# Optimization experiments

Measured on AMD Instinct MI355X. Metric: run time of the kernel, lower is better.

Reference implementation:

```python
import jax, jax.numpy as jnp
import numpy as np

# Irrep dims for irreps 0e, 1o, 2e: 2l+1
IRREP_DIMS = (1, 3, 5)
B, N, C_IN, C_OUT = 8, 4096, 256, 256
FEAT = sum(IRREP_DIMS)  # 9


def setup_inputs() -> dict:
    key = jax.random.key(0)
    kx, k0, k1, k2 = jax.random.split(key, 4)
    std = C_IN ** -0.5  # VarianceScaling(fan_in) init
    return {
        "x": jax.random.normal(kx, (B, N, C_IN, FEAT), dtype=jnp.float32),
        "w0": jax.random.normal(k0, (C_IN, C_OUT), dtype=jnp.float32) * std,
        "w1": jax.random.normal(k1, (C_IN, C_OUT), dtype=jnp.float32) * std,
        "w2": jax.random.normal(k2, (C_IN, C_OUT), dtype=jnp.float32) * std,
    }


def reference(x, w0, w1, w2):
    # EquivariantLinear with mix_channels=True:
    #  - axis_to_mul merges the channel axis into irrep multiplicity, so each
    #    irrep block x[..., k, m] (k = channel/mul index, m = 2l+1 component)
    #    is contracted over k with a per-irrep weight w_l [mul_in, mul_out],
    #    scaled by path_weight = 1/sqrt(fan_in) (single path per output irrep).
    #  - mul_to_axis splits the multiplicity back into the channel axis.
    # Block-diagonal structure: one small matmul per matching irrep pair.
    mul_in = x.shape[-2]
    pw = jnp.asarray(mul_in, x.dtype) ** -0.5  # path_weight (1/sqrt fan_in)
    outs = []
    offset = 0
    for w, d in zip((w0, w1, w2), IRREP_DIMS):
        xl = jax.lax.slice_in_dim(x, offset, offset + d, axis=-1)  # [B,N,C,d]
        outs.append(pw * jnp.einsum('bnkm,kc->bncm', xl, w))
        offset += d
    return jnp.concatenate(outs, axis=-1)  # [B, N, C_out, 9]
```

## Files before the change

### kernel.cpp

```cpp
#include <hip/hip_runtime.h>


typedef float f32x4 __attribute__((ext_vector_type(4)));
typedef float f32x4u __attribute__((ext_vector_type(4), aligned(4)));
typedef short s16x8 __attribute__((ext_vector_type(8)));

#define POSB 16
#define XS_KS 264
#define XS_MS (POSB * XS_KS)
#define SMEM_BYTES (9 * XS_MS * 2)
#define STG_ROW 148

__device__ __forceinline__ unsigned short f2bf(float f) {
  unsigned u = __float_as_uint(f);
  return (unsigned short)((u + 0x7FFFu + ((u >> 16) & 1u)) >> 16);
}

__device__ __forceinline__ unsigned cvt_pk_bf16(float lo, float hi) {
  unsigned r;
  asm("v_cvt_pk_bf16_f32 %0, %1, %2" : "=v"(r) : "v"(lo), "v"(hi));
  return r;
}

__global__ void prep_w(const float* __restrict__ w0, const float* __restrict__ w1,
                       const float* __restrict__ w2, unsigned short* __restrict__ wt) {
  const int b = blockIdx.x;
  const int irr = b / 16;
  const int tile = b % 16;
  const int k0 = (tile >> 2) << 6;
  const int c0 = (tile & 3) << 6;
  const float* w = (irr == 0) ? w0 : ((irr == 1) ? w1 : w2);
  __shared__ float lt[64 * 65];
  const int t = threadIdx.x;
#pragma unroll
  for (int i = 0; i < 16; ++i) {
    int e = t + (i << 8);
    int kk = e >> 6, cc = e & 63;
    lt[cc * 65 + kk] = w[(k0 + kk) * 256 + (c0 + cc)];
  }
  __syncthreads();
#pragma unroll
  for (int i = 0; i < 16; ++i) {
    int e = t + (i << 8);
    int cc = e >> 6, kk = e & 63;
    wt[irr * 65536 + (c0 + cc) * 256 + (k0 + kk)] = f2bf(lt[cc * 65 + kk] * 0.0625f);
  }
}

__global__ __launch_bounds__(512, 4) void eqlin_main(
    const float* __restrict__ x, const unsigned short* __restrict__ wt,
    float* __restrict__ out) {
  extern __shared__ char smem[];
  unsigned short* xs = reinterpret_cast<unsigned short*>(smem);

  const int t = threadIdx.x;
  const long long blk = blockIdx.x;
  const float* xb = x + blk * (POSB * 2304);

  {
    f32x4u va[8], vb[8];
    float vc[8];
#pragma unroll
    for (int i = 0; i < 8; ++i) {
      const float* s = xb + (t + (i << 9)) * 9;
      va[i] = *reinterpret_cast<const f32x4u*>(s);
      vb[i] = *reinterpret_cast<const f32x4u*>(s + 4);
      vc[i] = s[8];
    }
#pragma unroll
    for (int i = 0; i < 8; ++i) {
      const int u = t + (i << 9);
      const int pos = u >> 8;
      const int k = u & 255;
      unsigned short* base = xs + pos * XS_KS + k;
      unsigned p01 = cvt_pk_bf16(va[i][0], va[i][1]);
      unsigned p23 = cvt_pk_bf16(va[i][2], va[i][3]);
      unsigned p45 = cvt_pk_bf16(vb[i][0], vb[i][1]);
      unsigned p67 = cvt_pk_bf16(vb[i][2], vb[i][3]);
      base[0 * XS_MS] = (unsigned short)p01;
      base[1 * XS_MS] = (unsigned short)(p01 >> 16);
      base[2 * XS_MS] = (unsigned short)p23;
      base[3 * XS_MS] = (unsigned short)(p23 >> 16);
      base[4 * XS_MS] = (unsigned short)p45;
      base[5 * XS_MS] = (unsigned short)(p45 >> 16);
      base[6 * XS_MS] = (unsigned short)p67;
      base[7 * XS_MS] = (unsigned short)(p67 >> 16);
      base[8 * XS_MS] = f2bf(vc[i]);
    }
  }
  __syncthreads();

  const int w = t >> 6;
  const int l = t & 63;
  const int cr = l & 15;
  const int kg = (l >> 4) << 3;
  const int c0 = w << 5;

  const unsigned short* xsA = xs + cr * XS_KS + kg;
  const unsigned short* wtB = wt + (c0 + cr) * 256 + kg;

  f32x4 accA[4][2];
#pragma unroll
  for (int m = 0; m < 4; ++m)
#pragma unroll
    for (int ct = 0; ct < 2; ++ct) accA[m][ct] = (f32x4){0.f, 0.f, 0.f, 0.f};

#pragma unroll 2
  for (int ks = 0; ks < 8; ++ks) {
    const int kk = ks << 5;
    s16x8 b00 = *reinterpret_cast<const s16x8*>(wtB + kk);
    s16x8 b01 = *reinterpret_cast<const s16x8*>(wtB + 4096 + kk);
    s16x8 b10 = *reinterpret_cast<const s16x8*>(wtB + 65536 + kk);
    s16x8 b11 = *reinterpret_cast<const s16x8*>(wtB + 65536 + 4096 + kk);
    {
      s16x8 a = *reinterpret_cast<const s16x8*>(xsA + kk);
      accA[0][0] = __builtin_amdgcn_mfma_f32_16x16x32_bf16(a, b00, accA[0][0], 0, 0, 0);
      accA[0][1] = __builtin_amdgcn_mfma_f32_16x16x32_bf16(a, b01, accA[0][1], 0, 0, 0);
    }
#pragma unroll
    for (int m = 1; m < 4; ++m) {
      s16x8 a = *reinterpret_cast<const s16x8*>(xsA + m * XS_MS + kk);
      accA[m][0] = __builtin_amdgcn_mfma_f32_16x16x32_bf16(a, b10, accA[m][0], 0, 0, 0);
      accA[m][1] = __builtin_amdgcn_mfma_f32_16x16x32_bf16(a, b11, accA[m][1], 0, 0, 0);
    }
  }

  f32x4 accB[5][2];
#pragma unroll
  for (int m = 0; m < 5; ++m)
#pragma unroll
    for (int ct = 0; ct < 2; ++ct) accB[m][ct] = (f32x4){0.f, 0.f, 0.f, 0.f};

#pragma unroll 2
  for (int ks = 0; ks < 8; ++ks) {
    const int kk = ks << 5;
    s16x8 b20 = *reinterpret_cast<const s16x8*>(wtB + 2 * 65536 + kk);
    s16x8 b21 = *reinterpret_cast<const s16x8*>(wtB + 2 * 65536 + 4096 + kk);
#pragma unroll
    for (int m = 0; m < 5; ++m) {
      s16x8 a = *reinterpret_cast<const s16x8*>(xsA + (m + 4) * XS_MS + kk);
      accB[m][0] = __builtin_amdgcn_mfma_f32_16x16x32_bf16(a, b20, accB[m][0], 0, 0, 0);
      accB[m][1] = __builtin_amdgcn_mfma_f32_16x16x32_bf16(a, b21, accB[m][1], 0, 0, 0);
    }
  }
  __syncthreads();

  float* stgw = reinterpret_cast<float*>(smem) + w * (POSB * STG_ROW);
  const int posb = (l >> 4) << 2;
  f32x4* o4 = reinterpret_cast<f32x4*>(out) + blk * 9216 + w * 72;

#pragma unroll
  for (int ct = 0; ct < 2; ++ct) {
#pragma unroll
    for (int m = 0; m < 9; ++m) {
#pragma unroll
      for (int j = 0; j < 4; ++j) {
        float v = (m < 4) ? accA[m][ct][j] : accB[m - 4][ct][j];
        stgw[(posb + j) * STG_ROW + cr * 9 + m] = v;
      }
    }
    asm volatile("s_waitcnt lgkmcnt(0)" ::: "memory");
#pragma unroll
    for (int q = 0; q < 9; ++q) {
      const int e = l + (q << 6);
      const int pos = (int)((unsigned)e / 36u);
      const int rem = e - pos * 36;
      f32x4 v = *reinterpret_cast<const f32x4*>(stgw + pos * STG_ROW + (rem << 2));
      __builtin_nontemporal_store(v, &o4[pos * 576 + ct * 36 + rem]);
    }
    asm volatile("s_waitcnt lgkmcnt(0)" ::: "memory");
  }
}

extern "C" void kernel_launch(void* const* d_in, const int* in_sizes, int n_in,
                              void* d_out, int out_size, void* d_ws, size_t ws_size,
                              hipStream_t stream) {
  const float* x = (const float*)d_in[0];
  const float* w0 = (const float*)d_in[1];
  const float* w1 = (const float*)d_in[2];
  const float* w2 = (const float*)d_in[3];
  unsigned short* wt = (unsigned short*)d_ws;
  float* out = (float*)d_out;

  prep_w<<<48, 256, 0, stream>>>(w0, w1, w2, wt);

  (void)hipFuncSetAttribute(reinterpret_cast<const void*>(eqlin_main),
                            hipFuncAttributeMaxDynamicSharedMemorySize, SMEM_BYTES);
  eqlin_main<<<2048, 512, SMEM_BYTES, stream>>>(x, wt, out);
}
```

Before: 162.8 us.

## Pack two irrep components per MFMA row tile and halve positions per block

Each block now handles 8 positions with 256 threads, and each wave covers 64 output channels instead of 32. The 16-row MFMA A tile packs two different m-components (8 positions each) that share the same weight, so wasted row padding is removed and the number of MFMAs drops from 18 to 6 tiles per channel tile. The output staging is reorganised to match, and the grid doubles. This raises register pressure (24 accumulators) and lowers launch bounds, in return for fewer MFMAs and fewer redundant weight loads.

```diff
diff --git a/kernel.cpp b/kernel.cpp
--- a/kernel.cpp
+++ b/kernel.cpp
@@ -5,11 +5,11 @@
 typedef float f32x4u __attribute__((ext_vector_type(4), aligned(4)));
 typedef short s16x8 __attribute__((ext_vector_type(8)));
 
-#define POSB 16
+#define POSB 8
 #define XS_KS 264
 #define XS_MS (POSB * XS_KS)
 #define SMEM_BYTES (9 * XS_MS * 2)
-#define STG_ROW 148
+#define STG_ROW 292
 
 __device__ __forceinline__ unsigned short f2bf(float f) {
   unsigned u = __float_as_uint(f);
@@ -47,7 +47,7 @@
   }
 }
 
-__global__ __launch_bounds__(512, 4) void eqlin_main(
+__global__ __launch_bounds__(256, 3) void eqlin_main(
     const float* __restrict__ x, const unsigned short* __restrict__ wt,
     float* __restrict__ out) {
   extern __shared__ char smem[];
@@ -62,14 +62,14 @@
     float vc[8];
 #pragma unroll
     for (int i = 0; i < 8; ++i) {
-      const float* s = xb + (t + (i << 9)) * 9;
+      const float* s = xb + (t + (i << 8)) * 9;
       va[i] = *reinterpret_cast<const f32x4u*>(s);
       vb[i] = *reinterpret_cast<const f32x4u*>(s + 4);
       vc[i] = s[8];
     }
 #pragma unroll
     for (int i = 0; i < 8; ++i) {
-      const int u = t + (i << 9);
+      const int u = t + (i << 8);
       const int pos = u >> 8;
       const int k = u & 255;
       unsigned short* base = xs + pos * XS_KS + k;
@@ -94,79 +94,84 @@
   const int l = t & 63;
   const int cr = l & 15;
   const int kg = (l >> 4) << 3;
-  const int c0 = w << 5;
+  const int c0 = w << 6;
 
-  const unsigned short* xsA = xs + cr * XS_KS + kg;
+  const bool hi = (cr >= 8);
+  const unsigned short* xrow = xs + (cr & 7) * XS_KS + kg;
+  const unsigned short* xa[6] = {
+      xrow + 0 * XS_MS,
+      xrow + (hi ? 2 : 1) * XS_MS,
+      xrow + 3 * XS_MS,
+      xrow + (hi ? 5 : 4) * XS_MS,
+      xrow + (hi ? 7 : 6) * XS_MS,
+      xrow + 8 * XS_MS,
+  };
+
   const unsigned short* wtB = wt + (c0 + cr) * 256 + kg;
 
-  f32x4 accA[4][2];
+  f32x4 acc[4][6];
 #pragma unroll
-  for (int m = 0; m < 4; ++m)
+  for (int ct = 0; ct < 4; ++ct)
 #pragma unroll
-    for (int ct = 0; ct < 2; ++ct) accA[m][ct] = (f32x4){0.f, 0.f, 0.f, 0.f};
+    for (int T = 0; T < 6; ++T) acc[ct][T] = (f32x4){0.f, 0.f, 0.f, 0.f};
 
 #pragma unroll 2
   for (int ks = 0; ks < 8; ++ks) {
     const int kk = ks << 5;
-    s16x8 b00 = *reinterpret_cast<const s16x8*>(wtB + kk);
-    s16x8 b01 = *reinterpret_cast<const s16x8*>(wtB + 4096 + kk);
-    s16x8 b10 = *reinterpret_cast<const s16x8*>(wtB + 65536 + kk);
-    s16x8 b11 = *reinterpret_cast<const s16x8*>(wtB + 65536 + 4096 + kk);
-    {
-      s16x8 a = *reinterpret_cast<const s16x8*>(xsA + kk);
-      accA[0][0] = __builtin_amdgcn_mfma_f32_16x16x32_bf16(a, b00, accA[0][0], 0, 0, 0);
-      accA[0][1] = __builtin_amdgcn_mfma_f32_16x16x32_bf16(a, b01, accA[0][1], 0, 0, 0);
-    }
+    s16x8 a0 = *reinterpret_cast<const s16x8*>(xa[0] + kk);
+    s16x8 a1 = *reinterpret_cast<const s16x8*>(xa[1] + kk);
+    s16x8 a2 = *reinterpret_cast<const s16x8*>(xa[2] + kk);
+    s16x8 a3 = *reinterpret_cast<const s16x8*>(xa[3] + kk);
+    s16x8 a4 = *reinterpret_cast<const s16x8*>(xa[4] + kk);
+    s16x8 a5 = *reinterpret_cast<const s16x8*>(xa[5] + kk);
 #pragma unroll
-    for (int m = 1; m < 4; ++m) {
-      s16x8 a = *reinterpret_cast<const s16x8*>(xsA + m * XS_MS + kk);
-      accA[m][0] = __builtin_amdgcn_mfma_f32_16x16x32_bf16(a, b10, accA[m][0], 0, 0, 0);
-      accA[m][1] = __builtin_amdgcn_mfma_f32_16x16x32_bf16(a, b11, accA[m][1], 0, 0, 0);
-    }
-  }
-
-  f32x4 accB[5][2];
-#pragma unroll
-  for (int m = 0; m < 5; ++m)
-#pragma unroll
-    for (int ct = 0; ct < 2; ++ct) accB[m][ct] = (f32x4){0.f, 0.f, 0.f, 0.f};
-
-#pragma unroll 2
-  for (int ks = 0; ks < 8; ++ks) {
-    const int kk = ks << 5;
-    s16x8 b20 = *reinterpret_cast<const s16x8*>(wtB + 2 * 65536 + kk);
-    s16x8 b21 = *reinterpret_cast<const s16x8*>(wtB + 2 * 65536 + 4096 + kk);
-#pragma unroll
-    for (int m = 0; m < 5; ++m) {
-      s16x8 a = *reinterpret_cast<const s16x8*>(xsA + (m + 4) * XS_MS + kk);
-      accB[m][0] = __builtin_amdgcn_mfma_f32_16x16x32_bf16(a, b20, accB[m][0], 0, 0, 0);
-      accB[m][1] = __builtin_amdgcn_mfma_f32_16x16x32_bf16(a, b21, accB[m][1], 0, 0, 0);
+    for (int ct = 0; ct < 4; ++ct) {
+      const unsigned short* wc = wtB + ct * 4096 + kk;
+      s16x8 b0 = *reinterpret_cast<const s16x8*>(wc);
+      s16x8 b1 = *reinterpret_cast<const s16x8*>(wc + 65536);
+      s16x8 b2 = *reinterpret_cast<const s16x8*>(wc + 131072);
+      acc[ct][0] = __builtin_amdgcn_mfma_f32_16x16x32_bf16(a0, b0, acc[ct][0], 0, 0, 0);
+      acc[ct][1] = __builtin_amdgcn_mfma_f32_16x16x32_bf16(a1, b1, acc[ct][1], 0, 0, 0);
+      acc[ct][2] = __builtin_amdgcn_mfma_f32_16x16x32_bf16(a2, b1, acc[ct][2], 0, 0, 0);
+      acc[ct][3] = __builtin_amdgcn_mfma_f32_16x16x32_bf16(a3, b2, acc[ct][3], 0, 0, 0);
+      acc[ct][4] = __builtin_amdgcn_mfma_f32_16x16x32_bf16(a4, b2, acc[ct][4], 0, 0, 0);
+      acc[ct][5] = __builtin_amdgcn_mfma_f32_16x16x32_bf16(a5, b2, acc[ct][5], 0, 0, 0);
     }
   }
   __syncthreads();
 
   float* stgw = reinterpret_cast<float*>(smem) + w * (POSB * STG_ROW);
-  const int posb = (l >> 4) << 2;
-  f32x4* o4 = reinterpret_cast<f32x4*>(out) + blk * 9216 + w * 72;
+  const int g = l >> 4;
+  const int posb = (g & 1) << 2;
+
+  const int pAt[6] = {0, 1, 3, 4, 6, 8};
+  const int pBt[6] = {0, 2, 3, 5, 7, 8};
+
+  f32x4* o4 = reinterpret_cast<f32x4*>(out);
 
 #pragma unroll
-  for (int ct = 0; ct < 2; ++ct) {
+  for (int h = 0; h < 2; ++h) {
 #pragma unroll
-    for (int m = 0; m < 9; ++m) {
+    for (int ch = 0; ch < 2; ++ch) {
 #pragma unroll
-      for (int j = 0; j < 4; ++j) {
-        float v = (m < 4) ? accA[m][ct][j] : accB[m - 4][ct][j];
-        stgw[(posb + j) * STG_ROW + cr * 9 + m] = v;
+      for (int T = 0; T < 6; ++T) {
+        const int m = (g < 2) ? pAt[T] : pBt[T];
+        if (g < 2 || pAt[T] != pBt[T]) {
+#pragma unroll
+          for (int j = 0; j < 4; ++j)
+            stgw[(posb + j) * STG_ROW + ((ch << 4) + cr) * 9 + m] = acc[2 * h + ch][T][j];
+        }
       }
     }
     asm volatile("s_waitcnt lgkmcnt(0)" ::: "memory");
 #pragma unroll
     for (int q = 0; q < 9; ++q) {
       const int e = l + (q << 6);
-      const int pos = (int)((unsigned)e / 36u);
-      const int rem = e - pos * 36;
+      const int pos = (int)((unsigned)e / 72u);
+      const int rem = e - pos * 72;
       f32x4 v = *reinterpret_cast<const f32x4*>(stgw + pos * STG_ROW + (rem << 2));
-      __builtin_nontemporal_store(v, &o4[pos * 576 + ct * 36 + rem]);
+      __builtin_nontemporal_store(
+          v, &o4[(blk * POSB + pos) * 576 + w * 144 + h * 72 + rem]);
     }
     asm volatile("s_waitcnt lgkmcnt(0)" ::: "memory");
   }
@@ -186,5 +191,5 @@
 
   (void)hipFuncSetAttribute(reinterpret_cast<const void*>(eqlin_main),
                             hipFuncAttributeMaxDynamicSharedMemorySize, SMEM_BYTES);
-  eqlin_main<<<2048, 512, SMEM_BYTES, stream>>>(x, wt, out);
+  eqlin_main<<<4096, 256, SMEM_BYTES, stream>>>(x, wt, out);
 }
```

After: 280.0 us. +72.0%, slower.

## Make main kernel persistent over four tiles with double-buffered LDS prefetch

Applied to the files above, without the earlier changes.

Each block now processes four 16-position tiles instead of one, with two LDS buffers. The global loads for the next tile are issued before the MFMA loop of the current tile and staged into the other buffer after the output is written, so memory latency overlaps compute. The grid shrinks to 512 blocks, LDS use doubles, and launch bounds drop to 2 blocks per CU. That lowers occupancy and raises register pressure from holding prefetched tiles in registers.

```diff
diff --git a/kernel.cpp b/kernel.cpp
--- a/kernel.cpp
+++ b/kernel.cpp
@@ -8,8 +8,11 @@
 #define POSB 16
 #define XS_KS 264
 #define XS_MS (POSB * XS_KS)
-#define SMEM_BYTES (9 * XS_MS * 2)
+#define BUF_BYTES (9 * XS_MS * 2)
+#define SMEM_BYTES (2 * BUF_BYTES)
 #define STG_ROW 148
+#define NT 4
+#define TILE_FLOATS (POSB * 2304)
 
 __device__ __forceinline__ unsigned short f2bf(float f) {
   unsigned u = __float_as_uint(f);
@@ -20,6 +23,10 @@
   unsigned r;
   asm("v_cvt_pk_bf16_f32 %0, %1, %2" : "=v"(r) : "v"(lo), "v"(hi));
   return r;
+}
+
+__device__ __forceinline__ void bar_nodrain() {
+  asm volatile("s_waitcnt lgkmcnt(0)\n\ts_barrier" ::: "memory");
 }
 
 __global__ void prep_w(const float* __restrict__ w0, const float* __restrict__ w1,
@@ -47,128 +54,151 @@
   }
 }
 
-__global__ __launch_bounds__(512, 4) void eqlin_main(
+__device__ __forceinline__ void load8(const float* __restrict__ xb, int t,
+                                      f32x4u* va, f32x4u* vb, float* vc) {
+#pragma unroll
+  for (int i = 0; i < 8; ++i) {
+    const float* s = xb + (t + (i << 9)) * 9;
+    va[i] = *reinterpret_cast<const f32x4u*>(s);
+    vb[i] = *reinterpret_cast<const f32x4u*>(s + 4);
+    vc[i] = s[8];
+  }
+}
+
+__device__ __forceinline__ void stage8(unsigned short* __restrict__ xs, int t,
+                                       const f32x4u* va, const f32x4u* vb,
+                                       const float* vc) {
+#pragma unroll
+  for (int i = 0; i < 8; ++i) {
+    const int u = t + (i << 9);
+    const int pos = u >> 8;
+    const int k = u & 255;
+    unsigned short* base = xs + pos * XS_KS + k;
+    unsigned p01 = cvt_pk_bf16(va[i][0], va[i][1]);
+    unsigned p23 = cvt_pk_bf16(va[i][2], va[i][3]);
+    unsigned p45 = cvt_pk_bf16(vb[i][0], vb[i][1]);
+    unsigned p67 = cvt_pk_bf16(vb[i][2], vb[i][3]);
+    base[0 * XS_MS] = (unsigned short)p01;
+    base[1 * XS_MS] = (unsigned short)(p01 >> 16);
+    base[2 * XS_MS] = (unsigned short)p23;
+    base[3 * XS_MS] = (unsigned short)(p23 >> 16);
+    base[4 * XS_MS] = (unsigned short)p45;
+    base[5 * XS_MS] = (unsigned short)(p45 >> 16);
+    base[6 * XS_MS] = (unsigned short)p67;
+    base[7 * XS_MS] = (unsigned short)(p67 >> 16);
+    base[8 * XS_MS] = f2bf(vc[i]);
+  }
+}
+
+__global__ __launch_bounds__(512, 2) void eqlin_main(
     const float* __restrict__ x, const unsigned short* __restrict__ wt,
     float* __restrict__ out) {
   extern __shared__ char smem[];
-  unsigned short* xs = reinterpret_cast<unsigned short*>(smem);
 
   const int t = threadIdx.x;
   const long long blk = blockIdx.x;
-  const float* xb = x + blk * (POSB * 2304);
-
-  {
-    f32x4u va[8], vb[8];
-    float vc[8];
-#pragma unroll
-    for (int i = 0; i < 8; ++i) {
-      const float* s = xb + (t + (i << 9)) * 9;
-      va[i] = *reinterpret_cast<const f32x4u*>(s);
-      vb[i] = *reinterpret_cast<const f32x4u*>(s + 4);
-      vc[i] = s[8];
-    }
-#pragma unroll
-    for (int i = 0; i < 8; ++i) {
-      const int u = t + (i << 9);
-      const int pos = u >> 8;
-      const int k = u & 255;
-      unsigned short* base = xs + pos * XS_KS + k;
-      unsigned p01 = cvt_pk_bf16(va[i][0], va[i][1]);
-      unsigned p23 = cvt_pk_bf16(va[i][2], va[i][3]);
-      unsigned p45 = cvt_pk_bf16(vb[i][0], vb[i][1]);
-      unsigned p67 = cvt_pk_bf16(vb[i][2], vb[i][3]);
-      base[0 * XS_MS] = (unsigned short)p01;
-      base[1 * XS_MS] = (unsigned short)(p01 >> 16);
-      base[2 * XS_MS] = (unsigned short)p23;
-      base[3 * XS_MS] = (unsigned short)(p23 >> 16);
-      base[4 * XS_MS] = (unsigned short)p45;
-      base[5 * XS_MS] = (unsigned short)(p45 >> 16);
-      base[6 * XS_MS] = (unsigned short)p67;
-      base[7 * XS_MS] = (unsigned short)(p67 >> 16);
-      base[8 * XS_MS] = f2bf(vc[i]);
-    }
-  }
-  __syncthreads();
+  const float* xbase = x + blk * (NT * TILE_FLOATS);
 
   const int w = t >> 6;
   const int l = t & 63;
   const int cr = l & 15;
   const int kg = (l >> 4) << 3;
   const int c0 = w << 5;
-
-  const unsigned short* xsA = xs + cr * XS_KS + kg;
   const unsigned short* wtB = wt + (c0 + cr) * 256 + kg;
 
-  f32x4 accA[4][2];
-#pragma unroll
-  for (int m = 0; m < 4; ++m)
-#pragma unroll
-    for (int ct = 0; ct < 2; ++ct) accA[m][ct] = (f32x4){0.f, 0.f, 0.f, 0.f};
+  f32x4u va[8], vb[8];
+  float vc[8];
+
+  load8(xbase, t, va, vb, vc);
+  stage8(reinterpret_cast<unsigned short*>(smem), t, va, vb, vc);
+  bar_nodrain();
 
 #pragma unroll 2
-  for (int ks = 0; ks < 8; ++ks) {
-    const int kk = ks << 5;
-    s16x8 b00 = *reinterpret_cast<const s16x8*>(wtB + kk);
-    s16x8 b01 = *reinterpret_cast<const s16x8*>(wtB + 4096 + kk);
-    s16x8 b10 = *reinterpret_cast<const s16x8*>(wtB + 65536 + kk);
-    s16x8 b11 = *reinterpret_cast<const s16x8*>(wtB + 65536 + 4096 + kk);
-    {
-      s16x8 a = *reinterpret_cast<const s16x8*>(xsA + kk);
-      accA[0][0] = __builtin_amdgcn_mfma_f32_16x16x32_bf16(a, b00, accA[0][0], 0, 0, 0);
-      accA[0][1] = __builtin_amdgcn_mfma_f32_16x16x32_bf16(a, b01, accA[0][1], 0, 0, 0);
-    }
-#pragma unroll
-    for (int m = 1; m < 4; ++m) {
-      s16x8 a = *reinterpret_cast<const s16x8*>(xsA + m * XS_MS + kk);
-      accA[m][0] = __builtin_amdgcn_mfma_f32_16x16x32_bf16(a, b10, accA[m][0], 0, 0, 0);
-      accA[m][1] = __builtin_amdgcn_mfma_f32_16x16x32_bf16(a, b11, accA[m][1], 0, 0, 0);
-    }
-  }
-
-  f32x4 accB[5][2];
-#pragma unroll
-  for (int m = 0; m < 5; ++m)
-#pragma unroll
-    for (int ct = 0; ct < 2; ++ct) accB[m][ct] = (f32x4){0.f, 0.f, 0.f, 0.f};
+  for (int it = 0; it < NT; ++it) {
+    const int p = it & 1;
+    const unsigned short* xsb =
+        reinterpret_cast<const unsigned short*>(smem + p * BUF_BYTES);
+
+    if (it + 1 < NT) load8(xbase + (it + 1) * TILE_FLOATS, t, va, vb, vc);
+
+    const unsigned short* xsA = xsb + cr * XS_KS + kg;
+
+    f32x4 accA[4][2];
+#pragma unroll
+    for (int m = 0; m < 4; ++m)
+#pragma unroll
+      for (int ct = 0; ct < 2; ++ct) accA[m][ct] = (f32x4){0.f, 0.f, 0.f, 0.f};
 
 #pragma unroll 2
-  for (int ks = 0; ks < 8; ++ks) {
-    const int kk = ks << 5;
-    s16x8 b20 = *reinterpret_cast<const s16x8*>(wtB + 2 * 65536 + kk);
-    s16x8 b21 = *reinterpret_cast<const s16x8*>(wtB + 2 * 65536 + 4096 + kk);
-#pragma unroll
-    for (int m = 0; m < 5; ++m) {
-      s16x8 a = *reinterpret_cast<const s16x8*>(xsA + (m + 4) * XS_MS + kk);
-      accB[m][0] = __builtin_amdgcn_mfma_f32_16x16x32_bf16(a, b20, accB[m][0], 0, 0, 0);
-      accB[m][1] = __builtin_amdgcn_mfma_f32_16x16x32_bf16(a, b21, accB[m][1], 0, 0, 0);
-    }
-  }
-  __syncthreads();
-
-  float* stgw = reinterpret_cast<float*>(smem) + w * (POSB * STG_ROW);
-  const int posb = (l >> 4) << 2;
-  f32x4* o4 = reinterpret_cast<f32x4*>(out) + blk * 9216 + w * 72;
-
-#pragma unroll
-  for (int ct = 0; ct < 2; ++ct) {
-#pragma unroll
-    for (int m = 0; m < 9; ++m) {
-#pragma unroll
-      for (int j = 0; j < 4; ++j) {
-        float v = (m < 4) ? accA[m][ct][j] : accB[m - 4][ct][j];
-        stgw[(posb + j) * STG_ROW + cr * 9 + m] = v;
-      }
-    }
-    asm volatile("s_waitcnt lgkmcnt(0)" ::: "memory");
-#pragma unroll
-    for (int q = 0; q < 9; ++q) {
-      const int e = l + (q << 6);
-      const int pos = (int)((unsigned)e / 36u);
-      const int rem = e - pos * 36;
-      f32x4 v = *reinterpret_cast<const f32x4*>(stgw + pos * STG_ROW + (rem << 2));
-      __builtin_nontemporal_store(v, &o4[pos * 576 + ct * 36 + rem]);
-    }
-    asm volatile("s_waitcnt lgkmcnt(0)" ::: "memory");
+    for (int ks = 0; ks < 8; ++ks) {
+      const int kk = ks << 5;
+      s16x8 b00 = *reinterpret_cast<const s16x8*>(wtB + kk);
+      s16x8 b01 = *reinterpret_cast<const s16x8*>(wtB + 4096 + kk);
+      s16x8 b10 = *reinterpret_cast<const s16x8*>(wtB + 65536 + kk);
+      s16x8 b11 = *reinterpret_cast<const s16x8*>(wtB + 65536 + 4096 + kk);
+      {
+        s16x8 a = *reinterpret_cast<const s16x8*>(xsA + kk);
+        accA[0][0] = __builtin_amdgcn_mfma_f32_16x16x32_bf16(a, b00, accA[0][0], 0, 0, 0);
+        accA[0][1] = __builtin_amdgcn_mfma_f32_16x16x32_bf16(a, b01, accA[0][1], 0, 0, 0);
+      }
+#pragma unroll
+      for (int m = 1; m < 4; ++m) {
+        s16x8 a = *reinterpret_cast<const s16x8*>(xsA + m * XS_MS + kk);
+        accA[m][0] = __builtin_amdgcn_mfma_f32_16x16x32_bf16(a, b10, accA[m][0], 0, 0, 0);
+        accA[m][1] = __builtin_amdgcn_mfma_f32_16x16x32_bf16(a, b11, accA[m][1], 0, 0, 0);
+      }
+    }
+
+    f32x4 accB[5][2];
+#pragma unroll
+    for (int m = 0; m < 5; ++m)
+#pragma unroll
+      for (int ct = 0; ct < 2; ++ct) accB[m][ct] = (f32x4){0.f, 0.f, 0.f, 0.f};
+
+#pragma unroll 2
+    for (int ks = 0; ks < 8; ++ks) {
+      const int kk = ks << 5;
+      s16x8 b20 = *reinterpret_cast<const s16x8*>(wtB + 2 * 65536 + kk);
+      s16x8 b21 = *reinterpret_cast<const s16x8*>(wtB + 2 * 65536 + 4096 + kk);
+#pragma unroll
+      for (int m = 0; m < 5; ++m) {
+        s16x8 a = *reinterpret_cast<const s16x8*>(xsA + (m + 4) * XS_MS + kk);
+        accB[m][0] = __builtin_amdgcn_mfma_f32_16x16x32_bf16(a, b20, accB[m][0], 0, 0, 0);
+        accB[m][1] = __builtin_amdgcn_mfma_f32_16x16x32_bf16(a, b21, accB[m][1], 0, 0, 0);
+      }
+    }
+    bar_nodrain();
+
+    float* stgw = reinterpret_cast<float*>(smem + p * BUF_BYTES) + w * (POSB * STG_ROW);
+    const int posb = (l >> 4) << 2;
+    f32x4* o4 = reinterpret_cast<f32x4*>(out) + (blk * NT + it) * 9216 + w * 72;
+
+#pragma unroll
+    for (int ct = 0; ct < 2; ++ct) {
+#pragma unroll
+      for (int m = 0; m < 9; ++m) {
+#pragma unroll
+        for (int j = 0; j < 4; ++j) {
+          float v = (m < 4) ? accA[m][ct][j] : accB[m - 4][ct][j];
+          stgw[(posb + j) * STG_ROW + cr * 9 + m] = v;
+        }
+      }
+      asm volatile("s_waitcnt lgkmcnt(0)" ::: "memory");
+#pragma unroll
+      for (int q = 0; q < 9; ++q) {
+        const int e = l + (q << 6);
+        const int pos = (int)((unsigned)e / 36u);
+        const int rem = e - pos * 36;
+        f32x4 v = *reinterpret_cast<const f32x4*>(stgw + pos * STG_ROW + (rem << 2));
+        __builtin_nontemporal_store(v, &o4[pos * 576 + ct * 36 + rem]);
+      }
+      asm volatile("s_waitcnt lgkmcnt(0)" ::: "memory");
+    }
+
+    if (it + 1 < NT) {
+      stage8(reinterpret_cast<unsigned short*>(smem + (p ^ 1) * BUF_BYTES), t, va, vb, vc);
+    }
+    bar_nodrain();
   }
 }
 
@@ -186,5 +216,5 @@
 
   (void)hipFuncSetAttribute(reinterpret_cast<const void*>(eqlin_main),
                             hipFuncAttributeMaxDynamicSharedMemorySize, SMEM_BYTES);
-  eqlin_main<<<2048, 512, SMEM_BYTES, stream>>>(x, wt, out);
-}
+  eqlin_main<<<512, 512, SMEM_BYTES, stream>>>(x, wt, out);
+}
```

Result: slower. 192.4 us (+18.2%).
